# Optimization experiments

Hardware: AMD Instinct MI355X
Metric: run time of the kernel (lower is better)

Reference implementation:

```python
import jax, jax.numpy as jnp
import numpy as np

H_DIM = 64      # input_dim of edge_aggregation (== h_dim)
HID = 128       # hidden_size of each per-edge-type agg MLP
T = 5           # edge_types for non-nba dataset
B, E, N = 64, 1024, 512


def setup_inputs() -> dict:
    key = jax.random.key(0)
    ks = jax.random.split(key, 8)
    edge_distribution = jax.random.uniform(ks[0], (B, E, T), dtype=jnp.float32)
    H = jax.random.uniform(ks[1], (B, E, N), dtype=jnp.float32)
    ori = jax.random.normal(ks[2], (B, N, H_DIM), dtype=jnp.float32)
    s1 = 1.0 / np.sqrt(H_DIM)
    s2 = 1.0 / np.sqrt(HID)
    # stacked per-edge-type MLP params: Linear(64->128) -> ReLU -> Linear(128->64)
    W1 = jax.random.uniform(ks[3], (T, H_DIM, HID), minval=-s1, maxval=s1, dtype=jnp.float32)
    b1 = jax.random.uniform(ks[4], (T, HID), minval=-s1, maxval=s1, dtype=jnp.float32)
    W2 = jax.random.uniform(ks[5], (T, HID, H_DIM), minval=-s2, maxval=s2, dtype=jnp.float32)
    b2 = jax.random.uniform(ks[6], (T, H_DIM), minval=-s2, maxval=s2, dtype=jnp.float32)
    return {"edge_distribution": edge_distribution, "H": H, "ori": ori,
            "W1": W1, "b1": b1, "W2": W2, "b2": b2}


def reference(edge_distribution, H, ori, W1, b1, W2, b2):
    # incidence gather: hyperedge features [B, E, D]
    edges = jnp.matmul(H, ori)
    # per-edge-type 2-layer MLP, vectorized over the T edge types
    h = jax.nn.relu(jnp.einsum('bed,tdh->bteh', edges, W1) + b1[None, :, None, :])
    per_type = jnp.einsum('bteh,thd->bted', h, W2) + b2[None, :, None, :]
    # mixture-weighted sum over edge types -> [B, E, D]
    edge_feature = jnp.einsum('bet,bted->bed', edge_distribution, per_type)
    # scatter back through H^T and concat with original node features
    node_agg = jnp.einsum('ben,bed->bnd', H, edge_feature)  # H^T @ edge_feature
    node_feature = jnp.concatenate((node_agg, ori), axis=-1)  # [B, N, 2D]
    return node_feature
```

## Files before the change

### kernel.cpp

```cpp
#include <hip/hip_runtime.h>

#define B_   64
#define E_   1024
#define N_   512
#define D_   64
#define HID_ 128
#define T_   5

typedef __bf16 bf16x8 __attribute__((ext_vector_type(8)));
typedef float f32x4 __attribute__((ext_vector_type(4)));

__device__ __forceinline__ unsigned short f2bu(float f) {
    union { float f; unsigned int u; } v; v.f = f;
    unsigned int r = (v.u + 0x7fffu + ((v.u >> 16) & 1u)) >> 16;
    return (unsigned short)r;
}

__device__ __forceinline__ unsigned int pack2(float lo, float hi) {
    union { __bf16 b[2]; unsigned int u; } v;
    v.b[0] = (__bf16)lo; v.b[1] = (__bf16)hi;
    return v.u;
}

__device__ __forceinline__ uint4 cvt8(float4 a, float4 b) {
    union { __bf16 h[8]; uint4 u; } v;
    v.h[0] = (__bf16)a.x; v.h[1] = (__bf16)a.y; v.h[2] = (__bf16)a.z; v.h[3] = (__bf16)a.w;
    v.h[4] = (__bf16)b.x; v.h[5] = (__bf16)b.y; v.h[6] = (__bf16)b.z; v.h[7] = (__bf16)b.w;
    return v.u;
}

#define MFMA16(a, b, c) __builtin_amdgcn_mfma_f32_16x16x32_bf16((a), (b), (c), 0, 0, 0)

__global__ __launch_bounds__(256) void k_prep_w(const float* __restrict__ W1,
                                                const float* __restrict__ W2,
                                                unsigned short* __restrict__ W1T,
                                                unsigned short* __restrict__ W2T) {
    int idx = blockIdx.x * 256 + threadIdx.x;
    if (idx < T_ * HID_ * D_) {
        int t = idx / (HID_ * D_), rem = idx % (HID_ * D_);
        int h = rem / D_, d = rem % D_;
        W1T[idx] = f2bu(W1[(t * D_ + d) * HID_ + h]);
    } else {
        int j = idx - T_ * HID_ * D_;
        int t = j / (D_ * HID_), rem = j % (D_ * HID_);
        int d = rem / HID_, h = rem % HID_;
        W2T[j] = f2bu(W2[(t * HID_ + h) * D_ + d]);
    }
}

__global__ __launch_bounds__(256) void k_ori_prep(const float* __restrict__ ori,
                                                  float* __restrict__ out,
                                                  unsigned short* __restrict__ oriT) {
    int b = blockIdx.y, n0 = blockIdx.x * 64;
    __shared__ float tl[64 * 65];
    int tid = threadIdx.x;
    int dl = tid & 63;
    #pragma unroll 4
    for (int p = 0; p < 16; ++p) {
        int nn = p * 4 + (tid >> 6);
        float v = ori[(size_t)(b * N_ + n0 + nn) * D_ + dl];
        out[(size_t)(b * N_ + n0 + nn) * 128 + 64 + dl] = v;
        tl[dl * 65 + nn] = v;
    }
    __syncthreads();
    #pragma unroll 4
    for (int p = 0; p < 16; ++p) {
        int dd = p * 4 + (tid >> 6);
        oriT[(size_t)(b * D_ + dd) * N_ + n0 + dl] = f2bu(tl[dd * 65 + dl]);
    }
}

__global__ __launch_bounds__(256) void k_edge_mlp(const float* __restrict__ H,
                                                  const unsigned short* __restrict__ oriT,
                                                  const float* __restrict__ ed,
                                                  const float* __restrict__ b1,
                                                  const float* __restrict__ b2,
                                                  const unsigned short* __restrict__ W1T,
                                                  const unsigned short* __restrict__ W2T,
                                                  unsigned short* __restrict__ efT) {
    int bx = blockIdx.x;
    int b = bx >> 4, e0 = (bx & 15) * 64;
    __shared__ __align__(16) unsigned short aA[64 * 72];
    __shared__ __align__(16) unsigned short bB[64 * 72];
    __shared__ __align__(16) unsigned short a_sh[64 * 72];
    __shared__ __align__(16) unsigned short w_sh[128 * 72];
    __shared__ __align__(16) unsigned short h_sh[64 * 136];
    __shared__ float wd_sh[320];
    __shared__ float b1_sh[640];
    __shared__ float b2_sh[320];
    int tid = threadIdx.x, w = tid >> 6, l = tid & 63, q = l >> 4, c = l & 15;

    for (int u = tid; u < 320; u += 256) wd_sh[u] = ed[((size_t)b * E_ + e0) * T_ + u];
    for (int u = tid; u < 640; u += 256) b1_sh[u] = b1[u];
    for (int u = tid; u < 320; u += 256) b2_sh[u] = b2[u];

    const f32x4 zero = {0.f, 0.f, 0.f, 0.f};

    f32x4 acc1[4];
    #pragma unroll
    for (int fn = 0; fn < 4; ++fn) acc1[fn] = zero;

    for (int ks = 0; ks < 8; ++ks) {
        int k0 = ks * 64;
        #pragma unroll
        for (int p = 0; p < 2; ++p) {
            int u = p * 256 + tid, r = u >> 3, sg = u & 7;
            const float* s = &H[((size_t)b * E_ + e0 + r) * N_ + k0 + sg * 8];
            float4 f0 = *(const float4*)&s[0];
            float4 f1 = *(const float4*)&s[4];
            *(uint4*)&aA[r * 72 + sg * 8] = cvt8(f0, f1);
        }
        #pragma unroll
        for (int p = 0; p < 2; ++p) {
            int u = p * 256 + tid, r = u >> 3, sg = u & 7;
            *(uint4*)&bB[r * 72 + sg * 8] =
                *(const uint4*)&oriT[((size_t)b * D_ + r) * N_ + k0 + sg * 8];
        }
        __syncthreads();
        #pragma unroll
        for (int h = 0; h < 2; ++h) {
            bf16x8 a0 = *(const bf16x8*)&aA[(w * 16 + c) * 72 + h * 32 + q * 8];
            #pragma unroll
            for (int fn = 0; fn < 4; ++fn) {
                bf16x8 bb = *(const bf16x8*)&bB[(fn * 16 + c) * 72 + h * 32 + q * 8];
                acc1[fn] = MFMA16(a0, bb, acc1[fn]);
            }
        }
        __syncthreads();
    }
    #pragma unroll
    for (int fn = 0; fn < 4; ++fn)
        #pragma unroll
        for (int i = 0; i < 4; ++i)
            a_sh[(w * 16 + q * 4 + i) * 72 + fn * 16 + c] = f2bu(acc1[fn][i]);

    f32x4 y[4];
    #pragma unroll
    for (int fn = 0; fn < 4; ++fn) y[fn] = zero;

    for (int t = 0; t < T_; ++t) {
        __syncthreads();
        #pragma unroll
        for (int p = 0; p < 4; ++p) {
            int u = p * 256 + tid, hh = u >> 3, sg = u & 7;
            *(uint4*)&w_sh[hh * 72 + sg * 8] =
                *(const uint4*)&W1T[(t * HID_ + hh) * D_ + sg * 8];
        }
        __syncthreads();
        f32x4 hc[8];
        #pragma unroll
        for (int fn = 0; fn < 8; ++fn) hc[fn] = zero;
        #pragma unroll
        for (int ks = 0; ks < 2; ++ks) {
            bf16x8 a = *(const bf16x8*)&a_sh[(w * 16 + c) * 72 + ks * 32 + q * 8];
            #pragma unroll
            for (int fn = 0; fn < 8; ++fn) {
                bf16x8 bb = *(const bf16x8*)&w_sh[(fn * 16 + c) * 72 + ks * 32 + q * 8];
                hc[fn] = MFMA16(a, bb, hc[fn]);
            }
        }
        float wv[4];
        #pragma unroll
        for (int i = 0; i < 4; ++i) wv[i] = wd_sh[(w * 16 + q * 4 + i) * T_ + t];
        #pragma unroll
        for (int fn = 0; fn < 8; ++fn) {
            float b1v = b1_sh[t * HID_ + fn * 16 + c];
            #pragma unroll
            for (int i = 0; i < 4; ++i) {
                float v = hc[fn][i] + b1v;
                v = fmaxf(v, 0.0f) * wv[i];
                h_sh[(w * 16 + q * 4 + i) * 136 + fn * 16 + c] = f2bu(v);
            }
        }
        __syncthreads();
        #pragma unroll
        for (int p = 0; p < 4; ++p) {
            int u = p * 256 + tid, dd = u >> 4, sg = u & 15;
            *(uint4*)&w_sh[dd * 136 + sg * 8] =
                *(const uint4*)&W2T[(t * D_ + dd) * HID_ + sg * 8];
        }
        __syncthreads();
        #pragma unroll
        for (int ks = 0; ks < 4; ++ks) {
            bf16x8 a = *(const bf16x8*)&h_sh[(w * 16 + c) * 136 + ks * 32 + q * 8];
            #pragma unroll
            for (int fn = 0; fn < 4; ++fn) {
                bf16x8 bb = *(const bf16x8*)&w_sh[(fn * 16 + c) * 136 + ks * 32 + q * 8];
                y[fn] = MFMA16(a, bb, y[fn]);
            }
        }
    }
    #pragma unroll
    for (int fn = 0; fn < 4; ++fn) {
        int d = fn * 16 + c;
        ushort4 o;
        #pragma unroll
        for (int i = 0; i < 4; ++i) {
            int r = w * 16 + q * 4 + i;
            float s = y[fn][i];
            #pragma unroll
            for (int t = 0; t < T_; ++t) s += wd_sh[r * T_ + t] * b2_sh[t * D_ + d];
            ((unsigned short*)&o)[i] = f2bu(s);
        }
        *(ushort4*)&efT[((size_t)b * D_ + d) * E_ + e0 + w * 16 + q * 4] = o;
    }
}

__global__ __launch_bounds__(256) void k_gemm_out(const float* __restrict__ H,
                                                  const unsigned short* __restrict__ efT,
                                                  float* __restrict__ out) {
    int b = blockIdx.y, n0 = blockIdx.x * 64;
    __shared__ __align__(16) unsigned short aA[64 * 72];
    __shared__ unsigned int bB32[64 * 33];
    int tid = threadIdx.x, w = tid >> 6, l = tid & 63, q = l >> 4, c = l & 15;
    int r2 = tid >> 3, cg = tid & 7;
    const f32x4 zero = {0.f, 0.f, 0.f, 0.f};
    f32x4 acc[4];
    #pragma unroll
    for (int fm = 0; fm < 4; ++fm) acc[fm] = zero;

    for (int ks = 0; ks < 16; ++ks) {
        int k0 = ks * 64;
        #pragma unroll
        for (int p = 0; p < 2; ++p) {
            int u = p * 256 + tid, r = u >> 3, sg = u & 7;
            *(uint4*)&aA[r * 72 + sg * 8] =
                *(const uint4*)&efT[((size_t)b * D_ + r) * E_ + k0 + sg * 8];
        }
        {
            const float* s0 = &H[((size_t)b * E_ + k0 + 2 * r2) * N_ + n0 + cg * 8];
            const float* s1 = s0 + N_;
            float4 f0 = *(const float4*)&s0[0], f1 = *(const float4*)&s0[4];
            float4 g0 = *(const float4*)&s1[0], g1 = *(const float4*)&s1[4];
            float r0[8] = {f0.x, f0.y, f0.z, f0.w, f1.x, f1.y, f1.z, f1.w};
            float r1[8] = {g0.x, g0.y, g0.z, g0.w, g1.x, g1.y, g1.z, g1.w};
            #pragma unroll
            for (int j = 0; j < 8; ++j)
                bB32[(cg * 8 + j) * 33 + r2] = pack2(r0[j], r1[j]);
        }
        __syncthreads();
        #pragma unroll
        for (int h = 0; h < 2; ++h) {
            union { unsigned int u[4]; bf16x8 v; } bb;
            #pragma unroll
            for (int i = 0; i < 4; ++i)
                bb.u[i] = bB32[(w * 16 + c) * 33 + h * 16 + q * 4 + i];
            #pragma unroll
            for (int fm = 0; fm < 4; ++fm) {
                bf16x8 afr = *(const bf16x8*)&aA[(fm * 16 + c) * 72 + h * 32 + q * 8];
                acc[fm] = MFMA16(afr, bb.v, acc[fm]);
            }
        }
        __syncthreads();
    }
    #pragma unroll
    for (int fm = 0; fm < 4; ++fm) {
        *(f32x4*)&out[((size_t)b * N_ + n0 + w * 16 + c) * 128 + fm * 16 + q * 4] = acc[fm];
    }
}

extern "C" void kernel_launch(void* const* d_in, const int* in_sizes, int n_in,
                              void* d_out, int out_size, void* d_ws, size_t ws_size,
                              hipStream_t stream) {
    const float* ed  = (const float*)d_in[0];
    const float* H   = (const float*)d_in[1];
    const float* ori = (const float*)d_in[2];
    const float* W1  = (const float*)d_in[3];
    const float* b1  = (const float*)d_in[4];
    const float* W2  = (const float*)d_in[5];
    const float* b2  = (const float*)d_in[6];
    float* out = (float*)d_out;

    char* ws = (char*)d_ws;
    unsigned short* oriT = (unsigned short*)ws; ws += (size_t)B_ * D_ * N_ * 2;
    unsigned short* W1T  = (unsigned short*)ws; ws += (size_t)T_ * HID_ * D_ * 2;
    unsigned short* W2T  = (unsigned short*)ws; ws += (size_t)T_ * D_ * HID_ * 2;
    unsigned short* efT  = (unsigned short*)ws; ws += (size_t)B_ * D_ * E_ * 2;

    hipLaunchKernelGGL(k_prep_w, dim3(320), dim3(256), 0, stream, W1, W2, W1T, W2T);
    hipLaunchKernelGGL(k_ori_prep, dim3(8, 64), dim3(256), 0, stream, ori, out, oriT);
    hipLaunchKernelGGL(k_edge_mlp, dim3(1024), dim3(256), 0, stream,
                       H, oriT, ed, b1, b2, W1T, W2T, efT);
    hipLaunchKernelGGL(k_gemm_out, dim3(8, 64), dim3(256), 0, stream, H, efT, out);
}
```

Measured before the change: 277.6 us.

## Double-buffer LDS tiles with register prefetch and swizzle block order

Both GEMM kernels now prefetch the next K-slice from global memory into registers while MFMAs run on the current LDS buffer, using ping-pong shared buffers so each iteration needs one barrier instead of two. The MLP weight tiles for the next edge type are also prefetched into registers. Shared memory in k_edge_mlp is aliased into one buffer to keep LDS use down for a three-blocks-per-CU launch bound. Block indices are swizzled so concurrent blocks spread across batches. The costs are higher register pressure and doubled LDS in k_gemm_out.

```diff
diff --git a/kernel.cpp b/kernel.cpp
--- a/kernel.cpp
+++ b/kernel.cpp
@@ -70,25 +70,32 @@
     }
 }
 
-__global__ __launch_bounds__(256) void k_edge_mlp(const float* __restrict__ H,
-                                                  const unsigned short* __restrict__ oriT,
-                                                  const float* __restrict__ ed,
-                                                  const float* __restrict__ b1,
-                                                  const float* __restrict__ b2,
-                                                  const unsigned short* __restrict__ W1T,
-                                                  const unsigned short* __restrict__ W2T,
-                                                  unsigned short* __restrict__ efT) {
-    int bx = blockIdx.x;
+__global__ __launch_bounds__(256, 3) void k_edge_mlp(const float* __restrict__ H,
+                                                     const unsigned short* __restrict__ oriT,
+                                                     const float* __restrict__ ed,
+                                                     const float* __restrict__ b1,
+                                                     const float* __restrict__ b2,
+                                                     const unsigned short* __restrict__ W1T,
+                                                     const unsigned short* __restrict__ W2T,
+                                                     unsigned short* __restrict__ efT) {
+    int bid = blockIdx.x;
+    int bx = (bid & 7) * 128 + (bid >> 3);
     int b = bx >> 4, e0 = (bx & 15) * 64;
-    __shared__ __align__(16) unsigned short aA[64 * 72];
-    __shared__ __align__(16) unsigned short bB[64 * 72];
+    __shared__ __align__(16) unsigned short X[18432];
     __shared__ __align__(16) unsigned short a_sh[64 * 72];
-    __shared__ __align__(16) unsigned short w_sh[128 * 72];
-    __shared__ __align__(16) unsigned short h_sh[64 * 136];
     __shared__ float wd_sh[320];
     __shared__ float b1_sh[640];
     __shared__ float b2_sh[320];
     int tid = threadIdx.x, w = tid >> 6, l = tid & 63, q = l >> 4, c = l & 15;
+    int rs = tid >> 3, sgs = tid & 7;
+
+    uint4 w1r[4], w2r[4];
+    #pragma unroll
+    for (int p = 0; p < 4; ++p) {
+        int u2 = p * 256 + tid;
+        w1r[p] = *(const uint4*)&W1T[(u2 >> 3) * D_ + (u2 & 7) * 8];
+        w2r[p] = *(const uint4*)&W2T[(u2 >> 4) * HID_ + (u2 & 15) * 8];
+    }
 
     for (int u = tid; u < 320; u += 256) wd_sh[u] = ed[((size_t)b * E_ + e0) * T_ + u];
     for (int u = tid; u < 640; u += 256) b1_sh[u] = b1[u];
@@ -100,33 +107,59 @@
     #pragma unroll
     for (int fn = 0; fn < 4; ++fn) acc1[fn] = zero;
 
+    const float* Hb = &H[((size_t)b * E_ + e0) * N_];
+    const unsigned short* Ob = &oriT[(size_t)b * D_ * N_];
+
+    float4 f00, f01, f10, f11;
+    uint4 ob0, ob1;
+    {
+        const float* s0 = Hb + (size_t)rs * N_ + sgs * 8;
+        const float* s1 = Hb + (size_t)(rs + 32) * N_ + sgs * 8;
+        f00 = *(const float4*)&s0[0]; f01 = *(const float4*)&s0[4];
+        f10 = *(const float4*)&s1[0]; f11 = *(const float4*)&s1[4];
+        ob0 = *(const uint4*)&Ob[(size_t)rs * N_ + sgs * 8];
+        ob1 = *(const uint4*)&Ob[(size_t)(rs + 32) * N_ + sgs * 8];
+    }
+    {
+        unsigned short* aA = X;
+        unsigned short* bB = X + 4608;
+        *(uint4*)&aA[rs * 72 + sgs * 8] = cvt8(f00, f01);
+        *(uint4*)&aA[(rs + 32) * 72 + sgs * 8] = cvt8(f10, f11);
+        *(uint4*)&bB[rs * 72 + sgs * 8] = ob0;
+        *(uint4*)&bB[(rs + 32) * 72 + sgs * 8] = ob1;
+    }
+    __syncthreads();
+
     for (int ks = 0; ks < 8; ++ks) {
-        int k0 = ks * 64;
-        #pragma unroll
-        for (int p = 0; p < 2; ++p) {
-            int u = p * 256 + tid, r = u >> 3, sg = u & 7;
-            const float* s = &H[((size_t)b * E_ + e0 + r) * N_ + k0 + sg * 8];
-            float4 f0 = *(const float4*)&s[0];
-            float4 f1 = *(const float4*)&s[4];
-            *(uint4*)&aA[r * 72 + sg * 8] = cvt8(f0, f1);
-        }
-        #pragma unroll
-        for (int p = 0; p < 2; ++p) {
-            int u = p * 256 + tid, r = u >> 3, sg = u & 7;
-            *(uint4*)&bB[r * 72 + sg * 8] =
-                *(const uint4*)&oriT[((size_t)b * D_ + r) * N_ + k0 + sg * 8];
-        }
-        __syncthreads();
-        #pragma unroll
-        for (int h = 0; h < 2; ++h) {
-            bf16x8 a0 = *(const bf16x8*)&aA[(w * 16 + c) * 72 + h * 32 + q * 8];
+        if (ks < 7) {
+            int k0 = (ks + 1) * 64;
+            const float* s0 = Hb + (size_t)rs * N_ + k0 + sgs * 8;
+            const float* s1 = Hb + (size_t)(rs + 32) * N_ + k0 + sgs * 8;
+            f00 = *(const float4*)&s0[0]; f01 = *(const float4*)&s0[4];
+            f10 = *(const float4*)&s1[0]; f11 = *(const float4*)&s1[4];
+            ob0 = *(const uint4*)&Ob[(size_t)rs * N_ + k0 + sgs * 8];
+            ob1 = *(const uint4*)&Ob[(size_t)(rs + 32) * N_ + k0 + sgs * 8];
+        }
+        const unsigned short* aA = X + (ks & 1) * 9216;
+        const unsigned short* bB = aA + 4608;
+        #pragma unroll
+        for (int hh = 0; hh < 2; ++hh) {
+            bf16x8 a0 = *(const bf16x8*)&aA[(w * 16 + c) * 72 + hh * 32 + q * 8];
             #pragma unroll
             for (int fn = 0; fn < 4; ++fn) {
-                bf16x8 bb = *(const bf16x8*)&bB[(fn * 16 + c) * 72 + h * 32 + q * 8];
+                bf16x8 bb = *(const bf16x8*)&bB[(fn * 16 + c) * 72 + hh * 32 + q * 8];
                 acc1[fn] = MFMA16(a0, bb, acc1[fn]);
             }
         }
-        __syncthreads();
+        if (ks < 7) {
+            unsigned short* aN = X + ((ks & 1) ^ 1) * 9216;
+            unsigned short* bN = aN + 4608;
+            *(uint4*)&aN[rs * 72 + sgs * 8] = cvt8(f00, f01);
+            *(uint4*)&aN[(rs + 32) * 72 + sgs * 8] = cvt8(f10, f11);
+            *(uint4*)&bN[rs * 72 + sgs * 8] = ob0;
+            *(uint4*)&bN[(rs + 32) * 72 + sgs * 8] = ob1;
+            __syncthreads();
+        }
     }
     #pragma unroll
     for (int fn = 0; fn < 4; ++fn)
@@ -138,13 +171,22 @@
     #pragma unroll
     for (int fn = 0; fn < 4; ++fn) y[fn] = zero;
 
+    unsigned short* w_sh = X;
+    unsigned short* h_sh = X + 9216;
+
     for (int t = 0; t < T_; ++t) {
         __syncthreads();
         #pragma unroll
         for (int p = 0; p < 4; ++p) {
-            int u = p * 256 + tid, hh = u >> 3, sg = u & 7;
-            *(uint4*)&w_sh[hh * 72 + sg * 8] =
-                *(const uint4*)&W1T[(t * HID_ + hh) * D_ + sg * 8];
+            int u2 = p * 256 + tid;
+            *(uint4*)&w_sh[(u2 >> 3) * 72 + (u2 & 7) * 8] = w1r[p];
+        }
+        if (t < 4) {
+            #pragma unroll
+            for (int p = 0; p < 4; ++p) {
+                int u2 = p * 256 + tid;
+                w1r[p] = *(const uint4*)&W1T[((t + 1) * HID_ + (u2 >> 3)) * D_ + (u2 & 7) * 8];
+            }
         }
         __syncthreads();
         f32x4 hc[8];
@@ -175,9 +217,15 @@
         __syncthreads();
         #pragma unroll
         for (int p = 0; p < 4; ++p) {
-            int u = p * 256 + tid, dd = u >> 4, sg = u & 15;
-            *(uint4*)&w_sh[dd * 136 + sg * 8] =
-                *(const uint4*)&W2T[(t * D_ + dd) * HID_ + sg * 8];
+            int u2 = p * 256 + tid;
+            *(uint4*)&w_sh[(u2 >> 4) * 136 + (u2 & 15) * 8] = w2r[p];
+        }
+        if (t < 4) {
+            #pragma unroll
+            for (int p = 0; p < 4; ++p) {
+                int u2 = p * 256 + tid;
+                w2r[p] = *(const uint4*)&W2T[((t + 1) * D_ + (u2 >> 4)) * HID_ + (u2 & 15) * 8];
+            }
         }
         __syncthreads();
         #pragma unroll
@@ -209,9 +257,11 @@
 __global__ __launch_bounds__(256) void k_gemm_out(const float* __restrict__ H,
                                                   const unsigned short* __restrict__ efT,
                                                   float* __restrict__ out) {
-    int b = blockIdx.y, n0 = blockIdx.x * 64;
-    __shared__ __align__(16) unsigned short aA[64 * 72];
-    __shared__ unsigned int bB32[64 * 33];
+    int bid = blockIdx.x;
+    int swz = (bid & 7) * 64 + (bid >> 3);
+    int b = swz >> 3, n0 = (swz & 7) * 64;
+    __shared__ __align__(16) unsigned short aA[2][64 * 72];
+    __shared__ unsigned int bB32[2][64 * 33];
     int tid = threadIdx.x, w = tid >> 6, l = tid & 63, q = l >> 4, c = l & 15;
     int r2 = tid >> 3, cg = tid & 7;
     const f32x4 zero = {0.f, 0.f, 0.f, 0.f};
@@ -219,39 +269,64 @@
     #pragma unroll
     for (int fm = 0; fm < 4; ++fm) acc[fm] = zero;
 
+    const unsigned short* Ab = &efT[(size_t)b * D_ * E_];
+    const float* Hb = &H[(size_t)b * E_ * N_ + n0];
+
+    uint4 ar0, ar1;
+    float4 f0, f1, g0, g1;
+    {
+        ar0 = *(const uint4*)&Ab[(size_t)r2 * E_ + cg * 8];
+        ar1 = *(const uint4*)&Ab[(size_t)(r2 + 32) * E_ + cg * 8];
+        const float* s0 = Hb + (size_t)(2 * r2) * N_ + cg * 8;
+        const float* s1 = s0 + N_;
+        f0 = *(const float4*)&s0[0]; f1 = *(const float4*)&s0[4];
+        g0 = *(const float4*)&s1[0]; g1 = *(const float4*)&s1[4];
+    }
+    {
+        *(uint4*)&aA[0][r2 * 72 + cg * 8] = ar0;
+        *(uint4*)&aA[0][(r2 + 32) * 72 + cg * 8] = ar1;
+        float r0a[8] = {f0.x, f0.y, f0.z, f0.w, f1.x, f1.y, f1.z, f1.w};
+        float r1a[8] = {g0.x, g0.y, g0.z, g0.w, g1.x, g1.y, g1.z, g1.w};
+        #pragma unroll
+        for (int j = 0; j < 8; ++j)
+            bB32[0][(cg * 8 + j) * 33 + r2] = pack2(r0a[j], r1a[j]);
+    }
+    __syncthreads();
+
     for (int ks = 0; ks < 16; ++ks) {
-        int k0 = ks * 64;
-        #pragma unroll
-        for (int p = 0; p < 2; ++p) {
-            int u = p * 256 + tid, r = u >> 3, sg = u & 7;
-            *(uint4*)&aA[r * 72 + sg * 8] =
-                *(const uint4*)&efT[((size_t)b * D_ + r) * E_ + k0 + sg * 8];
-        }
-        {
-            const float* s0 = &H[((size_t)b * E_ + k0 + 2 * r2) * N_ + n0 + cg * 8];
+        if (ks < 15) {
+            int k0 = (ks + 1) * 64;
+            ar0 = *(const uint4*)&Ab[(size_t)r2 * E_ + k0 + cg * 8];
+            ar1 = *(const uint4*)&Ab[(size_t)(r2 + 32) * E_ + k0 + cg * 8];
+            const float* s0 = Hb + (size_t)(k0 + 2 * r2) * N_ + cg * 8;
             const float* s1 = s0 + N_;
-            float4 f0 = *(const float4*)&s0[0], f1 = *(const float4*)&s0[4];
-            float4 g0 = *(const float4*)&s1[0], g1 = *(const float4*)&s1[4];
-            float r0[8] = {f0.x, f0.y, f0.z, f0.w, f1.x, f1.y, f1.z, f1.w};
-            float r1[8] = {g0.x, g0.y, g0.z, g0.w, g1.x, g1.y, g1.z, g1.w};
+            f0 = *(const float4*)&s0[0]; f1 = *(const float4*)&s0[4];
+            g0 = *(const float4*)&s1[0]; g1 = *(const float4*)&s1[4];
+        }
+        int cur = ks & 1;
+        #pragma unroll
+        for (int hh = 0; hh < 2; ++hh) {
+            union { unsigned int u[4]; bf16x8 v; } bb;
+            #pragma unroll
+            for (int i = 0; i < 4; ++i)
+                bb.u[i] = bB32[cur][(w * 16 + c) * 33 + hh * 16 + q * 4 + i];
+            #pragma unroll
+            for (int fm = 0; fm < 4; ++fm) {
+                bf16x8 afr = *(const bf16x8*)&aA[cur][(fm * 16 + c) * 72 + hh * 32 + q * 8];
+                acc[fm] = MFMA16(afr, bb.v, acc[fm]);
+            }
+        }
+        if (ks < 15) {
+            int nxt = cur ^ 1;
+            *(uint4*)&aA[nxt][r2 * 72 + cg * 8] = ar0;
+            *(uint4*)&aA[nxt][(r2 + 32) * 72 + cg * 8] = ar1;
+            float r0a[8] = {f0.x, f0.y, f0.z, f0.w, f1.x, f1.y, f1.z, f1.w};
+            float r1a[8] = {g0.x, g0.y, g0.z, g0.w, g1.x, g1.y, g1.z, g1.w};
             #pragma unroll
             for (int j = 0; j < 8; ++j)
-                bB32[(cg * 8 + j) * 33 + r2] = pack2(r0[j], r1[j]);
-        }
-        __syncthreads();
-        #pragma unroll
-        for (int h = 0; h < 2; ++h) {
-            union { unsigned int u[4]; bf16x8 v; } bb;
-            #pragma unroll
-            for (int i = 0; i < 4; ++i)
-                bb.u[i] = bB32[(w * 16 + c) * 33 + h * 16 + q * 4 + i];
-            #pragma unroll
-            for (int fm = 0; fm < 4; ++fm) {
-                bf16x8 afr = *(const bf16x8*)&aA[(fm * 16 + c) * 72 + h * 32 + q * 8];
-                acc[fm] = MFMA16(afr, bb.v, acc[fm]);
-            }
-        }
-        __syncthreads();
+                bB32[nxt][(cg * 8 + j) * 33 + r2] = pack2(r0a[j], r1a[j]);
+            __syncthreads();
+        }
     }
     #pragma unroll
     for (int fm = 0; fm < 4; ++fm) {
@@ -281,5 +356,5 @@
     hipLaunchKernelGGL(k_ori_prep, dim3(8, 64), dim3(256), 0, stream, ori, out, oriT);
     hipLaunchKernelGGL(k_edge_mlp, dim3(1024), dim3(256), 0, stream,
                        H, oriT, ed, b1, b2, W1T, W2T, efT);
-    hipLaunchKernelGGL(k_gemm_out, dim3(8, 64), dim3(256), 0, stream, H, efT, out);
-}
+    hipLaunchKernelGGL(k_gemm_out, dim3(512), dim3(256), 0, stream, H, efT, out);
+}
```

After: 307.7 us. 10.8% more time.

## Double-buffer output GEMM, swizzle blocks, merge MLP weight loads to cut barriers

Applied to the files above, without the earlier changes.

k_gemm_out now prefetches the next K-tile of efT and H into registers while the current tile's MFMAs run, using ping-pong LDS buffers with one barrier per iteration. It also switches to a 1D grid with a swizzled block order. In k_edge_mlp, W1 and W2 are loaded together into a shared scratch region that aliases the GEMM staging buffers, which drops two barriers per edge type. The A fragments are now kept in registers across the edge-type loop. The cost is more registers and LDS in the output GEMM, which may lower occupancy.

```diff
diff --git a/kernel.cpp b/kernel.cpp
--- a/kernel.cpp
+++ b/kernel.cpp
@@ -80,10 +80,8 @@
                                                   unsigned short* __restrict__ efT) {
     int bx = blockIdx.x;
     int b = bx >> 4, e0 = (bx & 15) * 64;
-    __shared__ __align__(16) unsigned short aA[64 * 72];
-    __shared__ __align__(16) unsigned short bB[64 * 72];
+    __shared__ __align__(16) unsigned short X[17920];
     __shared__ __align__(16) unsigned short a_sh[64 * 72];
-    __shared__ __align__(16) unsigned short w_sh[128 * 72];
     __shared__ __align__(16) unsigned short h_sh[64 * 136];
     __shared__ float wd_sh[320];
     __shared__ float b1_sh[640];
@@ -96,6 +94,8 @@
 
     const f32x4 zero = {0.f, 0.f, 0.f, 0.f};
 
+    unsigned short* aA = X;
+    unsigned short* bB = X + 4608;
     f32x4 acc1[4];
     #pragma unroll
     for (int fn = 0; fn < 4; ++fn) acc1[fn] = zero;
@@ -128,35 +128,49 @@
         }
         __syncthreads();
     }
+
     #pragma unroll
     for (int fn = 0; fn < 4; ++fn)
         #pragma unroll
         for (int i = 0; i < 4; ++i)
             a_sh[(w * 16 + q * 4 + i) * 72 + fn * 16 + c] = f2bu(acc1[fn][i]);
 
+    bf16x8 afr[2];
+    #pragma unroll
+    for (int ks = 0; ks < 2; ++ks)
+        afr[ks] = *(const bf16x8*)&a_sh[(w * 16 + c) * 72 + ks * 32 + q * 8];
+
+    unsigned short* w1_sh = X;
+    unsigned short* w2_sh = X + 9216;
+
     f32x4 y[4];
     #pragma unroll
     for (int fn = 0; fn < 4; ++fn) y[fn] = zero;
 
     for (int t = 0; t < T_; ++t) {
+        #pragma unroll
+        for (int p = 0; p < 4; ++p) {
+            int u2 = p * 256 + tid, hh = u2 >> 3, sg = u2 & 7;
+            *(uint4*)&w1_sh[hh * 72 + sg * 8] =
+                *(const uint4*)&W1T[((size_t)t * HID_ + hh) * D_ + sg * 8];
+        }
+        #pragma unroll
+        for (int p = 0; p < 4; ++p) {
+            int u2 = p * 256 + tid, dd = u2 >> 4, sg = u2 & 15;
+            *(uint4*)&w2_sh[dd * 136 + sg * 8] =
+                *(const uint4*)&W2T[((size_t)t * D_ + dd) * HID_ + sg * 8];
+        }
         __syncthreads();
-        #pragma unroll
-        for (int p = 0; p < 4; ++p) {
-            int u = p * 256 + tid, hh = u >> 3, sg = u & 7;
-            *(uint4*)&w_sh[hh * 72 + sg * 8] =
-                *(const uint4*)&W1T[(t * HID_ + hh) * D_ + sg * 8];
-        }
-        __syncthreads();
+
         f32x4 hc[8];
         #pragma unroll
         for (int fn = 0; fn < 8; ++fn) hc[fn] = zero;
         #pragma unroll
         for (int ks = 0; ks < 2; ++ks) {
-            bf16x8 a = *(const bf16x8*)&a_sh[(w * 16 + c) * 72 + ks * 32 + q * 8];
             #pragma unroll
             for (int fn = 0; fn < 8; ++fn) {
-                bf16x8 bb = *(const bf16x8*)&w_sh[(fn * 16 + c) * 72 + ks * 32 + q * 8];
-                hc[fn] = MFMA16(a, bb, hc[fn]);
+                bf16x8 bb = *(const bf16x8*)&w1_sh[(fn * 16 + c) * 72 + ks * 32 + q * 8];
+                hc[fn] = MFMA16(afr[ks], bb, hc[fn]);
             }
         }
         float wv[4];
@@ -172,24 +186,18 @@
                 h_sh[(w * 16 + q * 4 + i) * 136 + fn * 16 + c] = f2bu(v);
             }
         }
-        __syncthreads();
-        #pragma unroll
-        for (int p = 0; p < 4; ++p) {
-            int u = p * 256 + tid, dd = u >> 4, sg = u & 15;
-            *(uint4*)&w_sh[dd * 136 + sg * 8] =
-                *(const uint4*)&W2T[(t * D_ + dd) * HID_ + sg * 8];
-        }
-        __syncthreads();
         #pragma unroll
         for (int ks = 0; ks < 4; ++ks) {
             bf16x8 a = *(const bf16x8*)&h_sh[(w * 16 + c) * 136 + ks * 32 + q * 8];
             #pragma unroll
             for (int fn = 0; fn < 4; ++fn) {
-                bf16x8 bb = *(const bf16x8*)&w_sh[(fn * 16 + c) * 136 + ks * 32 + q * 8];
+                bf16x8 bb = *(const bf16x8*)&w2_sh[(fn * 16 + c) * 136 + ks * 32 + q * 8];
                 y[fn] = MFMA16(a, bb, y[fn]);
             }
         }
-    }
+        if (t < T_ - 1) __syncthreads();
+    }
+
     #pragma unroll
     for (int fn = 0; fn < 4; ++fn) {
         int d = fn * 16 + c;
@@ -209,9 +217,11 @@
 __global__ __launch_bounds__(256) void k_gemm_out(const float* __restrict__ H,
                                                   const unsigned short* __restrict__ efT,
                                                   float* __restrict__ out) {
-    int b = blockIdx.y, n0 = blockIdx.x * 64;
-    __shared__ __align__(16) unsigned short aA[64 * 72];
-    __shared__ unsigned int bB32[64 * 33];
+    int bid = blockIdx.x;
+    int swz = (bid & 7) * 64 + (bid >> 3);
+    int b = swz >> 3, n0 = (swz & 7) * 64;
+    __shared__ __align__(16) unsigned short aA[2][64 * 72];
+    __shared__ unsigned int bB32[2][64 * 33];
     int tid = threadIdx.x, w = tid >> 6, l = tid & 63, q = l >> 4, c = l & 15;
     int r2 = tid >> 3, cg = tid & 7;
     const f32x4 zero = {0.f, 0.f, 0.f, 0.f};
@@ -219,39 +229,64 @@
     #pragma unroll
     for (int fm = 0; fm < 4; ++fm) acc[fm] = zero;
 
+    const unsigned short* Ab = &efT[(size_t)b * D_ * E_];
+    const float* Hb = &H[(size_t)b * E_ * N_ + n0];
+
+    uint4 ar0, ar1;
+    float4 f0, f1, g0, g1;
+    {
+        ar0 = *(const uint4*)&Ab[(size_t)r2 * E_ + cg * 8];
+        ar1 = *(const uint4*)&Ab[(size_t)(r2 + 32) * E_ + cg * 8];
+        const float* s0 = Hb + (size_t)(2 * r2) * N_ + cg * 8;
+        const float* s1 = s0 + N_;
+        f0 = *(const float4*)&s0[0]; f1 = *(const float4*)&s0[4];
+        g0 = *(const float4*)&s1[0]; g1 = *(const float4*)&s1[4];
+    }
+    {
+        *(uint4*)&aA[0][r2 * 72 + cg * 8] = ar0;
+        *(uint4*)&aA[0][(r2 + 32) * 72 + cg * 8] = ar1;
+        float r0a[8] = {f0.x, f0.y, f0.z, f0.w, f1.x, f1.y, f1.z, f1.w};
+        float r1a[8] = {g0.x, g0.y, g0.z, g0.w, g1.x, g1.y, g1.z, g1.w};
+        #pragma unroll
+        for (int j = 0; j < 8; ++j)
+            bB32[0][(cg * 8 + j) * 33 + r2] = pack2(r0a[j], r1a[j]);
+    }
+    __syncthreads();
+
     for (int ks = 0; ks < 16; ++ks) {
-        int k0 = ks * 64;
-        #pragma unroll
-        for (int p = 0; p < 2; ++p) {
-            int u = p * 256 + tid, r = u >> 3, sg = u & 7;
-            *(uint4*)&aA[r * 72 + sg * 8] =
-                *(const uint4*)&efT[((size_t)b * D_ + r) * E_ + k0 + sg * 8];
-        }
-        {
-            const float* s0 = &H[((size_t)b * E_ + k0 + 2 * r2) * N_ + n0 + cg * 8];
+        if (ks < 15) {
+            int k0 = (ks + 1) * 64;
+            ar0 = *(const uint4*)&Ab[(size_t)r2 * E_ + k0 + cg * 8];
+            ar1 = *(const uint4*)&Ab[(size_t)(r2 + 32) * E_ + k0 + cg * 8];
+            const float* s0 = Hb + (size_t)(k0 + 2 * r2) * N_ + cg * 8;
             const float* s1 = s0 + N_;
-            float4 f0 = *(const float4*)&s0[0], f1 = *(const float4*)&s0[4];
-            float4 g0 = *(const float4*)&s1[0], g1 = *(const float4*)&s1[4];
-            float r0[8] = {f0.x, f0.y, f0.z, f0.w, f1.x, f1.y, f1.z, f1.w};
-            float r1[8] = {g0.x, g0.y, g0.z, g0.w, g1.x, g1.y, g1.z, g1.w};
+            f0 = *(const float4*)&s0[0]; f1 = *(const float4*)&s0[4];
+            g0 = *(const float4*)&s1[0]; g1 = *(const float4*)&s1[4];
+        }
+        int cur = ks & 1;
+        #pragma unroll
+        for (int hh = 0; hh < 2; ++hh) {
+            union { unsigned int u[4]; bf16x8 v; } bb;
+            #pragma unroll
+            for (int i = 0; i < 4; ++i)
+                bb.u[i] = bB32[cur][(w * 16 + c) * 33 + hh * 16 + q * 4 + i];
+            #pragma unroll
+            for (int fm = 0; fm < 4; ++fm) {
+                bf16x8 afr = *(const bf16x8*)&aA[cur][(fm * 16 + c) * 72 + hh * 32 + q * 8];
+                acc[fm] = MFMA16(afr, bb.v, acc[fm]);
+            }
+        }
+        if (ks < 15) {
+            int nxt = cur ^ 1;
+            *(uint4*)&aA[nxt][r2 * 72 + cg * 8] = ar0;
+            *(uint4*)&aA[nxt][(r2 + 32) * 72 + cg * 8] = ar1;
+            float r0a[8] = {f0.x, f0.y, f0.z, f0.w, f1.x, f1.y, f1.z, f1.w};
+            float r1a[8] = {g0.x, g0.y, g0.z, g0.w, g1.x, g1.y, g1.z, g1.w};
             #pragma unroll
             for (int j = 0; j < 8; ++j)
-                bB32[(cg * 8 + j) * 33 + r2] = pack2(r0[j], r1[j]);
-        }
-        __syncthreads();
-        #pragma unroll
-        for (int h = 0; h < 2; ++h) {
-            union { unsigned int u[4]; bf16x8 v; } bb;
-            #pragma unroll
-            for (int i = 0; i < 4; ++i)
-                bb.u[i] = bB32[(w * 16 + c) * 33 + h * 16 + q * 4 + i];
-            #pragma unroll
-            for (int fm = 0; fm < 4; ++fm) {
-                bf16x8 afr = *(const bf16x8*)&aA[(fm * 16 + c) * 72 + h * 32 + q * 8];
-                acc[fm] = MFMA16(afr, bb.v, acc[fm]);
-            }
-        }
-        __syncthreads();
+                bB32[nxt][(cg * 8 + j) * 33 + r2] = pack2(r0a[j], r1a[j]);
+            __syncthreads();
+        }
     }
     #pragma unroll
     for (int fm = 0; fm < 4; ++fm) {
@@ -281,5 +316,5 @@
     hipLaunchKernelGGL(k_ori_prep, dim3(8, 64), dim3(256), 0, stream, ori, out, oriT);
     hipLaunchKernelGGL(k_edge_mlp, dim3(1024), dim3(256), 0, stream,
                        H, oriT, ed, b1, b2, W1T, W2T, efT);
-    hipLaunchKernelGGL(k_gemm_out, dim3(8, 64), dim3(256), 0, stream, H, efT, out);
-}
+    hipLaunchKernelGGL(k_gemm_out, dim3(512), dim3(256), 0, stream, H, efT, out);
+}
```

Result: faster. 267.2 us (-3.8%).

## Fuse scatter GEMM into edge MLP kernel with atomic accumulation

Applied to the files above, without the earlier changes.

Removes the separate output GEMM kernel. Each edge block now multiplies its edge-feature tile, kept in shared memory, by its own H rows and atomically adds partial node sums into the output. The output is zeroed in the ori prep kernel. This avoids writing and re-reading the bf16 edge-feature buffer and the second full pass over H. The cost is many float atomics and nondeterministic summation order. The first GEMM's shared tiles also move to an XOR-swizzled layout without padding.

```diff
diff --git a/kernel.cpp b/kernel.cpp
--- a/kernel.cpp
+++ b/kernel.cpp
@@ -60,6 +60,7 @@
         int nn = p * 4 + (tid >> 6);
         float v = ori[(size_t)(b * N_ + n0 + nn) * D_ + dl];
         out[(size_t)(b * N_ + n0 + nn) * 128 + 64 + dl] = v;
+        out[(size_t)(b * N_ + n0 + nn) * 128 + dl] = 0.0f;
         tl[dl * 65 + nn] = v;
     }
     __syncthreads();
@@ -77,11 +78,10 @@
                                                   const float* __restrict__ b2,
                                                   const unsigned short* __restrict__ W1T,
                                                   const unsigned short* __restrict__ W2T,
-                                                  unsigned short* __restrict__ efT) {
+                                                  float* __restrict__ out) {
     int bx = blockIdx.x;
     int b = bx >> 4, e0 = (bx & 15) * 64;
-    __shared__ __align__(16) unsigned short aA[64 * 72];
-    __shared__ __align__(16) unsigned short bB[64 * 72];
+    __shared__ __align__(16) unsigned short X[8832];
     __shared__ __align__(16) unsigned short a_sh[64 * 72];
     __shared__ __align__(16) unsigned short w_sh[128 * 72];
     __shared__ __align__(16) unsigned short h_sh[64 * 136];
@@ -89,6 +89,8 @@
     __shared__ float b1_sh[640];
     __shared__ float b2_sh[320];
     int tid = threadIdx.x, w = tid >> 6, l = tid & 63, q = l >> 4, c = l & 15;
+    int rs = tid >> 3, sgs = tid & 7;
+    int swsl = (sgs ^ (rs & 7)) * 8;
 
     for (int u = tid; u < 320; u += 256) wd_sh[u] = ed[((size_t)b * E_ + e0) * T_ + u];
     for (int u = tid; u < 640; u += 256) b1_sh[u] = b1[u];
@@ -100,29 +102,31 @@
     #pragma unroll
     for (int fn = 0; fn < 4; ++fn) acc1[fn] = zero;
 
+    const float* Hb = &H[((size_t)b * E_ + e0) * N_];
+    const unsigned short* Ob = &oriT[(size_t)b * D_ * N_];
+    unsigned short* aA = X;
+    unsigned short* bB = X + 4096;
+
     for (int ks = 0; ks < 8; ++ks) {
         int k0 = ks * 64;
-        #pragma unroll
-        for (int p = 0; p < 2; ++p) {
-            int u = p * 256 + tid, r = u >> 3, sg = u & 7;
-            const float* s = &H[((size_t)b * E_ + e0 + r) * N_ + k0 + sg * 8];
-            float4 f0 = *(const float4*)&s[0];
-            float4 f1 = *(const float4*)&s[4];
-            *(uint4*)&aA[r * 72 + sg * 8] = cvt8(f0, f1);
-        }
-        #pragma unroll
-        for (int p = 0; p < 2; ++p) {
-            int u = p * 256 + tid, r = u >> 3, sg = u & 7;
-            *(uint4*)&bB[r * 72 + sg * 8] =
-                *(const uint4*)&oriT[((size_t)b * D_ + r) * N_ + k0 + sg * 8];
-        }
-        __syncthreads();
-        #pragma unroll
-        for (int h = 0; h < 2; ++h) {
-            bf16x8 a0 = *(const bf16x8*)&aA[(w * 16 + c) * 72 + h * 32 + q * 8];
+        const float* s0 = Hb + (size_t)rs * N_ + k0 + sgs * 8;
+        const float* s1 = Hb + (size_t)(rs + 32) * N_ + k0 + sgs * 8;
+        float4 f00 = *(const float4*)&s0[0], f01 = *(const float4*)&s0[4];
+        float4 f10 = *(const float4*)&s1[0], f11 = *(const float4*)&s1[4];
+        *(uint4*)&aA[rs * 64 + swsl] = cvt8(f00, f01);
+        *(uint4*)&aA[(rs + 32) * 64 + swsl] = cvt8(f10, f11);
+        *(uint4*)&bB[rs * 64 + swsl] =
+            *(const uint4*)&Ob[(size_t)rs * N_ + k0 + sgs * 8];
+        *(uint4*)&bB[(rs + 32) * 64 + swsl] =
+            *(const uint4*)&Ob[(size_t)(rs + 32) * N_ + k0 + sgs * 8];
+        __syncthreads();
+        #pragma unroll
+        for (int hh = 0; hh < 2; ++hh) {
+            int sl = ((hh * 4 + q) ^ (c & 7)) * 8;
+            bf16x8 a0 = *(const bf16x8*)&aA[(w * 16 + c) * 64 + sl];
             #pragma unroll
             for (int fn = 0; fn < 4; ++fn) {
-                bf16x8 bb = *(const bf16x8*)&bB[(fn * 16 + c) * 72 + h * 32 + q * 8];
+                bf16x8 bb = *(const bf16x8*)&bB[(fn * 16 + c) * 64 + sl];
                 acc1[fn] = MFMA16(a0, bb, acc1[fn]);
             }
         }
@@ -190,72 +194,60 @@
             }
         }
     }
+
+    unsigned short* ef_sh = X;
+    unsigned int* bB32 = (unsigned int*)(X + 4608);
     #pragma unroll
     for (int fn = 0; fn < 4; ++fn) {
         int d = fn * 16 + c;
-        ushort4 o;
         #pragma unroll
         for (int i = 0; i < 4; ++i) {
             int r = w * 16 + q * 4 + i;
             float s = y[fn][i];
             #pragma unroll
             for (int t = 0; t < T_; ++t) s += wd_sh[r * T_ + t] * b2_sh[t * D_ + d];
-            ((unsigned short*)&o)[i] = f2bu(s);
-        }
-        *(ushort4*)&efT[((size_t)b * D_ + d) * E_ + e0 + w * 16 + q * 4] = o;
-    }
-}
-
-__global__ __launch_bounds__(256) void k_gemm_out(const float* __restrict__ H,
-                                                  const unsigned short* __restrict__ efT,
-                                                  float* __restrict__ out) {
-    int b = blockIdx.y, n0 = blockIdx.x * 64;
-    __shared__ __align__(16) unsigned short aA[64 * 72];
-    __shared__ unsigned int bB32[64 * 33];
-    int tid = threadIdx.x, w = tid >> 6, l = tid & 63, q = l >> 4, c = l & 15;
+            ef_sh[d * 72 + r] = f2bu(s);
+        }
+    }
+    __syncthreads();
+
     int r2 = tid >> 3, cg = tid & 7;
-    const f32x4 zero = {0.f, 0.f, 0.f, 0.f};
-    f32x4 acc[4];
-    #pragma unroll
-    for (int fm = 0; fm < 4; ++fm) acc[fm] = zero;
-
-    for (int ks = 0; ks < 16; ++ks) {
-        int k0 = ks * 64;
-        #pragma unroll
-        for (int p = 0; p < 2; ++p) {
-            int u = p * 256 + tid, r = u >> 3, sg = u & 7;
-            *(uint4*)&aA[r * 72 + sg * 8] =
-                *(const uint4*)&efT[((size_t)b * D_ + r) * E_ + k0 + sg * 8];
-        }
+    for (int ks = 0; ks < 8; ++ks) {
+        int n0 = ks * 64;
         {
-            const float* s0 = &H[((size_t)b * E_ + k0 + 2 * r2) * N_ + n0 + cg * 8];
+            const float* s0 = &H[((size_t)b * E_ + e0 + 2 * r2) * N_ + n0 + cg * 8];
             const float* s1 = s0 + N_;
             float4 f0 = *(const float4*)&s0[0], f1 = *(const float4*)&s0[4];
             float4 g0 = *(const float4*)&s1[0], g1 = *(const float4*)&s1[4];
-            float r0[8] = {f0.x, f0.y, f0.z, f0.w, f1.x, f1.y, f1.z, f1.w};
-            float r1[8] = {g0.x, g0.y, g0.z, g0.w, g1.x, g1.y, g1.z, g1.w};
+            float r0a[8] = {f0.x, f0.y, f0.z, f0.w, f1.x, f1.y, f1.z, f1.w};
+            float r1a[8] = {g0.x, g0.y, g0.z, g0.w, g1.x, g1.y, g1.z, g1.w};
             #pragma unroll
             for (int j = 0; j < 8; ++j)
-                bB32[(cg * 8 + j) * 33 + r2] = pack2(r0[j], r1[j]);
-        }
-        __syncthreads();
-        #pragma unroll
-        for (int h = 0; h < 2; ++h) {
+                bB32[(cg * 8 + j) * 33 + r2] = pack2(r0a[j], r1a[j]);
+        }
+        __syncthreads();
+        f32x4 acc3[4];
+        #pragma unroll
+        for (int fm = 0; fm < 4; ++fm) acc3[fm] = zero;
+        #pragma unroll
+        for (int hh = 0; hh < 2; ++hh) {
             union { unsigned int u[4]; bf16x8 v; } bb;
             #pragma unroll
             for (int i = 0; i < 4; ++i)
-                bb.u[i] = bB32[(w * 16 + c) * 33 + h * 16 + q * 4 + i];
+                bb.u[i] = bB32[(w * 16 + c) * 33 + hh * 16 + q * 4 + i];
             #pragma unroll
             for (int fm = 0; fm < 4; ++fm) {
-                bf16x8 afr = *(const bf16x8*)&aA[(fm * 16 + c) * 72 + h * 32 + q * 8];
-                acc[fm] = MFMA16(afr, bb.v, acc[fm]);
-            }
-        }
-        __syncthreads();
-    }
-    #pragma unroll
-    for (int fm = 0; fm < 4; ++fm) {
-        *(f32x4*)&out[((size_t)b * N_ + n0 + w * 16 + c) * 128 + fm * 16 + q * 4] = acc[fm];
+                bf16x8 afr = *(const bf16x8*)&ef_sh[(fm * 16 + c) * 72 + hh * 32 + q * 8];
+                acc3[fm] = MFMA16(afr, bb.v, acc3[fm]);
+            }
+        }
+        float* op = &out[((size_t)b * N_ + n0 + w * 16 + c) * 128];
+        #pragma unroll
+        for (int fm = 0; fm < 4; ++fm)
+            #pragma unroll
+            for (int i = 0; i < 4; ++i)
+                atomicAdd(&op[fm * 16 + q * 4 + i], acc3[fm][i]);
+        if (ks < 7) __syncthreads();
     }
 }
 
@@ -272,14 +264,13 @@
     float* out = (float*)d_out;
 
     char* ws = (char*)d_ws;
-    unsigned short* oriT = (unsigned short*)ws; ws += (size_t)B_ * D_ * N_ * 2;
-    unsigned short* W1T  = (unsigned short*)ws; ws += (size_t)T_ * HID_ * D_ * 2;
-    unsigned short* W2T  = (unsigned short*)ws; ws += (size_t)T_ * D_ * HID_ * 2;
-    unsigned short* efT  = (unsigned short*)ws; ws += (size_t)B_ * D_ * E_ * 2;
+    size_t used = 0;
+    unsigned short* oriT = (unsigned short*)(ws + used); used += (size_t)B_ * D_ * N_ * 2;
+    unsigned short* W1T  = (unsigned short*)(ws + used); used += (size_t)T_ * HID_ * D_ * 2;
+    unsigned short* W2T  = (unsigned short*)(ws + used); used += (size_t)T_ * D_ * HID_ * 2;
 
     hipLaunchKernelGGL(k_prep_w, dim3(320), dim3(256), 0, stream, W1, W2, W1T, W2T);
     hipLaunchKernelGGL(k_ori_prep, dim3(8, 64), dim3(256), 0, stream, ori, out, oriT);
     hipLaunchKernelGGL(k_edge_mlp, dim3(1024), dim3(256), 0, stream,
-                       H, oriT, ed, b1, b2, W1T, W2T, efT);
-    hipLaunchKernelGGL(k_gemm_out, dim3(8, 64), dim3(256), 0, stream, H, efT, out);
-}
+                       H, oriT, ed, b1, b2, W1T, W2T, out);
+}
```

Measured after the change: 620.0 us. 123% more time.
